# Performance work log

Hardware: AMD Instinct MI355X
Metric: run time of the kernel (lower is better)

Reference implementation:

```python
import jax, jax.numpy as jnp
import numpy as np

# Screen config (matches init_kwargs)
W, H, TL = 1920, 1080, 16
NBW = -(-W // TL)          # 120
NBH = -(-H // TL)          # 68
NB = NBW * NBH             # 8160 tiles
N = 500_000                # number of points
K = 5                      # max tiles per axis a point can overlap (radius < 24, TL=16)
RADIUS_MAX = 24.0


def setup_inputs() -> dict:
    key = jax.random.key(0)
    k1, k2, k3 = jax.random.split(key, 3)
    pos2d = jax.random.uniform(k1, (N, 2), dtype=jnp.float32) * jnp.array([W, H], dtype=jnp.float32)
    radius = jax.random.uniform(k2, (N,), dtype=jnp.float32) * (RADIUS_MAX - 1.0) + 1.0
    depth = jax.random.normal(k3, (N,), dtype=jnp.float32)
    return {"pos2d": pos2d, "radius": radius, "depth": depth}


def reference(pos2d, radius, depth):
    # Tile bounds per point (identical clamping semantics to the torch module).
    xmin = jnp.clip(jnp.floor_divide(pos2d[:, 0] - radius, TL), 0, NBW).astype(jnp.int32)
    ymin = jnp.clip(jnp.floor_divide(pos2d[:, 1] - radius, TL), 0, NBH).astype(jnp.int32)
    xmax = jnp.clip(jnp.floor_divide(pos2d[:, 0] + radius, TL) + 1, 0, NBW).astype(jnp.int32)
    ymax = jnp.clip(jnp.floor_divide(pos2d[:, 1] + radius, TL) + 1, 0, NBH).astype(jnp.int32)

    # Enumerate a fixed KxK candidate tile window per point, mask out-of-range tiles.
    dxy = jnp.arange(K, dtype=jnp.int32)
    xi = xmin[:, None] + dxy            # [N, K]
    yi = ymin[:, None] + dxy            # [N, K]
    vx = xi < xmax[:, None]
    vy = yi < ymax[:, None]
    valid = (vx[:, :, None] & vy[:, None, :]).reshape(-1)              # [E]
    tid = (xi[:, :, None] * NBH + yi[:, None, :]).reshape(-1)          # [E] flat tile id (x-major, as in module)
    tid = jnp.where(valid, tid, NB).astype(jnp.int32)                  # sentinel NB -> sorts to end
    pid = jnp.broadcast_to(jnp.arange(N, dtype=jnp.int32)[:, None, None], (N, K, K)).reshape(-1)
    d_entry = jnp.broadcast_to(depth[:, None, None], (N, K, K)).reshape(-1)

    # Counting-sort equivalent: per-tile histogram + exclusive cumsum offsets.
    counts = jax.ops.segment_sum(valid.astype(jnp.int32), tid, num_segments=NB + 1)[:NB]
    tile_count = jnp.concatenate([jnp.zeros((1,), jnp.int32), jnp.cumsum(counts)[:-1].astype(jnp.int32)])

    # Sort pairs by (tile id, depth descending) -> contiguous per-tile, depth-sorted index lists.
    order = jnp.lexsort((-d_entry, tid))
    tid_s = tid[order]
    pid_s = pid[order]
    live = tid_s < NB
    tile_indices = jnp.where(live, pid_s, -1)                          # padded with -1 at the tail
    sorted_depth = jnp.where(live, depth[pid_s], 0.0)                  # depths in per-tile sorted order
    return tile_count, tile_indices, sorted_depth
```

## Files before the change

### kernel.cpp

```cpp
#include <hip/hip_runtime.h>
#include <stdint.h>
#include <math.h>

typedef unsigned short u16;
typedef unsigned int u32;
typedef unsigned long long u64;

#define NBW 120
#define NBH 68
#define NTILES (NBW * NBH)
#define NPTS 500000
#define EE 12500000
#define SORT_CAP 768
#define NBKT 512
#define CAP 128
#define SLABF (NTILES * CAP * 2)
#define HB2 256
#define HT2 1024
#define RD_CH 8
#define RD_WB 17
#define DX 121
#define DY 69
#define DCELLS 8352
#define DCW (DCELLS / 2)

__device__ __forceinline__ int clampi(int v, int lo, int hi) {
    return v < lo ? lo : (v > hi ? hi : v);
}

__device__ __forceinline__ void tile_window(float x, float y, float r,
                                            int& x0, int& x1, int& y0, int& y1) {
    x0 = clampi((int)floorf((x - r) * 0.0625f), 0, NBW);
    x1 = clampi((int)floorf((x + r) * 0.0625f) + 1, 0, NBW);
    y0 = clampi((int)floorf((y - r) * 0.0625f), 0, NBH);
    y1 = clampi((int)floorf((y + r) * 0.0625f) + 1, 0, NBH);
}

__device__ __forceinline__ u32 depth_key(float d) {
    u32 fu = __float_as_uint(d);
    u32 asc = (fu & 0x80000000u) ? ~fu : (fu | 0x80000000u);
    return ~asc;
}
__device__ __forceinline__ float depth_unkey(u32 dk) {
    u32 asc = ~dk;
    u32 fu = (asc & 0x80000000u) ? (asc & 0x7FFFFFFFu) : ~asc;
    return __uint_as_float(fu);
}

__device__ __forceinline__ int tile_of_block(int b) {
    return (b & 7) * (NTILES / 8) + (b >> 3);
}

__device__ __forceinline__ u32 bucket_of(u32 dk, const u32* __restrict__ Ts) {
    u32 k = dk >> 24;
    u32 t0 = Ts[k], t1 = Ts[k + 1];
    u32 b = t0 + (((t1 - t0) * ((dk >> 8) & 0xFFFFu)) >> 16);
    return b >= NBKT ? (NBKT - 1) : b;
}

__device__ __forceinline__ void lds_inc16(u32* arr, int cell) {
    atomicAdd(&arr[cell >> 1], (cell & 1) ? 0x10000u : 1u);
}


__global__ void zero_kernel(u32* __restrict__ cnt, int* __restrict__ sdg) {
    int i = blockIdx.x * 1024 + threadIdx.x;
    if (i < NTILES) cnt[i] = 0;
    int j = i - NTILES;
    if (j >= 0 && j < DCELLS) sdg[j] = 0;
}

__global__ __launch_bounds__(HT2) void scatter_hist_kernel(const float2* __restrict__ pos,
                                                           const float* __restrict__ rad,
                                                           const float* __restrict__ depth,
                                                           u32* __restrict__ cnt,
                                                           u64* __restrict__ slab,
                                                           u32* __restrict__ diffslc) {
    __shared__ u32 s_dp[DCW];
    __shared__ u32 s_dm[DCW];
    int tid = threadIdx.x;
    for (int w = tid; w < DCW; w += HT2) { s_dp[w] = 0; s_dm[w] = 0; }
    __syncthreads();

    for (int i = blockIdx.x * HT2 + tid; i < NPTS; i += HB2 * HT2) {
        float2 p = pos[i];
        float r = rad[i];
        int x0, x1, y0, y1;
        tile_window(p.x, p.y, r, x0, x1, y0, y1);
        int cx = (int)(p.x * 0.0625f);
        int cy = (int)(p.y * 0.0625f);
        u32 dk = depth_key(depth[i]);
        u32 meta = ((u32)(cx - x0) << 11) | ((u32)(x1 - cx - 1) << 9)
                 | ((u32)y0 << 2) | (u32)(y1 - y0 - 1);
        int ct = cx * NBH + cy;
        u32 slot = atomicAdd(&cnt[ct], 1u);
        if (slot < CAP)
            slab[(size_t)ct * CAP + slot] = ((u64)dk << 32) | ((u64)(u32)i << 13) | (u64)meta;
        lds_inc16(s_dp, x0 * DY + y0);
        lds_inc16(s_dp, x1 * DY + y1);
        lds_inc16(s_dm, x0 * DY + y1);
        lds_inc16(s_dm, x1 * DY + y0);
    }
    __syncthreads();

    for (int wi = tid; wi < DCW; wi += HT2) {
        u32 pw = s_dp[wi], mw = s_dm[wi];
        int d0 = (int)(pw & 0xFFFFu) - (int)(mw & 0xFFFFu);
        int d1 = (int)(pw >> 16)     - (int)(mw >> 16);
        diffslc[blockIdx.x * DCW + wi] = ((u32)d0 & 0xFFFFu) | ((u32)d1 << 16);
    }
}

__global__ void reduce_diff_kernel(const u32* __restrict__ diffslc, int* __restrict__ sdg) {
    int chunk = blockIdx.x / RD_WB;
    int wb    = blockIdx.x % RD_WB;
    int wi = wb * 256 + threadIdx.x;
    if (wi >= DCW) return;
    int a0 = 0, a1 = 0;
    int b0 = chunk * (HB2 / RD_CH);
    for (int b = b0; b < b0 + HB2 / RD_CH; ++b) {
        u32 w = diffslc[b * DCW + wi];
        a0 += (int)(short)(w & 0xFFFFu);
        a1 += (int)(short)(w >> 16);
    }
    atomicAdd(&sdg[2 * wi],     a0);
    atomicAdd(&sdg[2 * wi + 1], a1);
}

__global__ __launch_bounds__(1024) void scan2_kernel(const int* __restrict__ sdg,
                                                     u32* __restrict__ eo,
                                                     float* __restrict__ out_count,
                                                     u32* __restrict__ Tg) {
    __shared__ int sd[DCELLS];
    __shared__ u32 wsum16[16];
    __shared__ u32 wpre[17];
    __shared__ u32 traw[257];
    int t = threadIdx.x;
    int lane = t & 63;
    int wvid = t >> 6;

    if (blockIdx.x == 0) {
        for (int c = t; c < DCELLS; c += 1024) sd[c] = sdg[c];
        __syncthreads();

        for (int x = wvid; x < DX; x += 16) {
            int idx = x * DY + lane;
            int v = sd[idx];
            for (int off = 1; off < 64; off <<= 1) {
                int n = __shfl_up(v, off, 64);
                if (lane >= off) v += n;
            }
            sd[idx] = v;
            int carry = __shfl(v, 63, 64);
            int y2 = 64 + lane;
            int v2 = (y2 < DY) ? sd[x * DY + y2] : 0;
            for (int off = 1; off < 64; off <<= 1) {
                int n = __shfl_up(v2, off, 64);
                if (lane >= off) v2 += n;
            }
            if (y2 < DY) sd[x * DY + y2] = v2 + carry;
        }
        __syncthreads();

        for (int y = wvid; y < DY; y += 16) {
            int idx = lane * DY + y;
            int v = sd[idx];
            for (int off = 1; off < 64; off <<= 1) {
                int n = __shfl_up(v, off, 64);
                if (lane >= off) v += n;
            }
            sd[idx] = v;
            int carry = __shfl(v, 63, 64);
            int x2 = 64 + lane;
            int v2 = (x2 < DX) ? sd[x2 * DY + y] : 0;
            for (int off = 1; off < 64; off <<= 1) {
                int n = __shfl_up(v2, off, 64);
                if (lane >= off) v2 += n;
            }
            if (x2 < DX) sd[x2 * DY + y] = v2 + carry;
        }
        __syncthreads();

        int base = t * 8;
        u32 local[8]; u32 sum = 0;
#pragma unroll
        for (int j = 0; j < 8; ++j) {
            int idx = base + j;
            u32 c = 0;
            if (idx < NTILES) {
                int x = idx / NBH, y = idx % NBH;
                c = (u32)sd[x * DY + y];
            }
            local[j] = c; sum += c;
        }
        u32 v = sum;
        for (int off = 1; off < 64; off <<= 1) {
            u32 n = __shfl_up(v, off, 64);
            if (lane >= off) v += n;
        }
        if (lane == 63) wsum16[wvid] = v;
        __syncthreads();
        if (t == 0) {
            u32 run = 0;
            wpre[0] = 0;
#pragma unroll
            for (int w = 0; w < 16; ++w) { run += wsum16[w]; wpre[w + 1] = run; }
        }
        __syncthreads();
        u32 run = wpre[wvid] + v - sum;
#pragma unroll
        for (int j = 0; j < 8; ++j) {
            int idx = base + j;
            if (idx < NTILES) {
                eo[idx] = run;
                out_count[idx] = (float)run;
                run += local[j];
            }
        }
        if (t == 1023) eo[NTILES] = wpre[16];
    } else {
        if (t < 257) {
            u32 dkb = (u32)t << 24;
            float d = depth_unkey(dkb);
            float u;
            if (d != d) u = (t < 128) ? 0.f : 1.f;
            else {
                float dc = fminf(fmaxf(d, -12.f), 12.f);
                u = 0.5f * erfcf(dc * 0.70710678f);
            }
            traw[t] = (u32)(u * (float)NBKT + 0.5f);
        }
        __syncthreads();
        if (t == 0) {
            u32 run = 0;
            for (int k = 0; k < 257; ++k) {
                u32 v = traw[k];
                if (v > NBKT) v = NBKT;
                if (v > run) run = v;
                Tg[k] = run;
            }
        }
    }
}

__global__ __launch_bounds__(256) void tile_build_kernel(const u32* __restrict__ cnt,
                                                         const u64* __restrict__ slab,
                                                         const u32* __restrict__ eo,
                                                         const u32* __restrict__ Tg,
                                                         float* __restrict__ out_idx,
                                                         float* __restrict__ out_depth) {
    __shared__ u64 keys[SORT_CAP];
    __shared__ u64 keys2[SORT_CAP];
    __shared__ u32 boff[NBKT + 1];
    __shared__ u32 bcur[NBKT];
    __shared__ u32 Ts[257];
    __shared__ u32 wsum[4];
    __shared__ u32 lcnt;
    __shared__ u32 nb_n[25];
    __shared__ u32 nb_base[25];
    __shared__ int nb_dcx[25];

    int tid = threadIdx.x;
    int lane = tid & 63;
    int wv = tid >> 6;

    {
        u32 total = eo[NTILES];
        u32 tailn = EE - total;
        u32 per = (tailn + NTILES - 1) / NTILES;
        u64 s = (u64)total + (u64)blockIdx.x * per;
        u64 e = s + per; if (e > (u64)EE) e = EE;
        for (u64 i = s + tid; i < e; i += 256) out_idx[i] = -1.f;

        u32 limit = EE - SLABF;
        u32 tn2 = limit > total ? limit - total : 0;
        u32 per2 = (tn2 + NTILES - 1) / NTILES;
        u64 s2 = (u64)total + (u64)blockIdx.x * per2;
        u64 e2 = s2 + per2; if (e2 > (u64)limit) e2 = limit;
        for (u64 i = s2 + tid; i < e2; i += 256) out_depth[i] = 0.f;
    }

    int t = tile_of_block(blockIdx.x);
    u32 base = eo[t];
    int cnt_e = (int)(eo[t + 1] - base);
    if (cnt_e <= 0) return;

    int tx = t / NBH;
    int ty = t % NBH;
    bool big = cnt_e > SORT_CAP;

    for (int b = tid; b < NBKT; b += 256) boff[b] = 0;
    for (int k = tid; k < 257; k += 256) Ts[k] = Tg[k];
    if (tid == 0) lcnt = 0;
    if (tid < 25) {
        int dx = tid / 5 - 2, dy = tid % 5 - 2;
        int ncx = tx + dx, ncy = ty + dy;
        u32 n = 0, b = 0;
        if (ncx >= 0 && ncx < NBW && ncy >= 0 && ncy < NBH) {
            int nt = ncx * NBH + ncy;
            n = cnt[nt]; if (n > CAP) n = CAP;
            b = (u32)nt * CAP;
        }
        nb_base[tid] = b;
        nb_dcx[tid] = dx;
        nb_n[tid] = n;
    }
    __syncthreads();

    if (!big) {
        for (int k = wv; k < 25; k += 4) {
            u32 n = nb_n[k];
            if (!n) continue;
            const u64* sp = slab + nb_base[k];
            int dcx = nb_dcx[k];
            for (u32 j0 = 0; j0 < n; j0 += 64) {
                u32 j = j0 + lane;
                bool acc = false;
                u64 v = 0;
                if (j < n) {
                    v = sp[j];
                    u32 meta = (u32)v & 0x1FFFu;
                    int h = (int)(meta & 3u);
                    int y0 = (int)((meta >> 2) & 127u);
                    int dx1m1 = (int)((meta >> 9) & 3u);
                    int dx0 = (int)((meta >> 11) & 3u);
                    acc = (dx0 >= dcx && dx1m1 >= -dcx && ty >= y0 && ty <= y0 + h);
                }
                u64 mask = __ballot(acc);
                if (!mask) continue;
                int leader = __ffsll((unsigned long long)mask) - 1;
                u32 nacc = (u32)__popcll(mask);
                u32 wbase = 0;
                if (lane == leader) wbase = atomicAdd(&lcnt, nacc);
                wbase = __shfl(wbase, leader, 64);
                if (acc) {
                    u32 rank = (u32)__popcll(mask & ((1ull << lane) - 1ull));
                    keys[wbase + rank] = v;
                    atomicAdd(&boff[bucket_of((u32)(v >> 32), Ts)], 1u);
                }
            }
        }
        __syncthreads();

        {
            int b0 = tid * 2;
            u32 h0 = boff[b0], h1 = boff[b0 + 1];
            u32 tsum = h0 + h1;
            u32 v = tsum;
            for (int off = 1; off < 64; off <<= 1) {
                u32 n = __shfl_up(v, off, 64);
                if (lane >= off) v += n;
            }
            if (lane == 63) wsum[wv] = v;
            __syncthreads();
            u32 wpre = 0;
            for (int w = 0; w < wv; ++w) wpre += wsum[w];
            u32 run = wpre + v - tsum;
            boff[b0] = run;     bcur[b0] = run;     run += h0;
            boff[b0 + 1] = run; bcur[b0 + 1] = run; run += h1;
            if (tid == 255) boff[NBKT] = run;
        }
        __syncthreads();

        for (int i = tid; i < cnt_e; i += 256) {
            u64 v = keys[i];
            u32 slot = atomicAdd(&bcur[bucket_of((u32)(v >> 32), Ts)], 1u);
            keys2[slot] = v;
        }
        __syncthreads();

        for (int b = tid; b < NBKT; b += 256) {
            int s = (int)boff[b], e = (int)boff[b + 1];
            for (int i = s + 1; i < e; ++i) {
                u64 k = keys2[i];
                int j = i - 1;
                while (j >= s && keys2[j] > k) { keys2[j + 1] = keys2[j]; --j; }
                keys2[j + 1] = k;
            }
        }
        __syncthreads();

        for (int i = tid; i < cnt_e; i += 256) {
            u64 k = keys2[i];
            u32 pid = (u32)(k >> 13) & 0x7FFFFu;
            u32 dk  = (u32)(k >> 32);
            out_idx[base + i]   = (float)pid;
            out_depth[base + i] = depth_unkey(dk);
        }
    } else {
        for (int k = wv; k < 25; k += 4) {
            u32 n = nb_n[k];
            if (!n) continue;
            const u64* sp = slab + nb_base[k];
            int dcx = nb_dcx[k];
            for (u32 j = lane; j < n; j += 64) {
                u64 v = sp[j];
                u32 meta = (u32)v & 0x1FFFu;
                int h = (int)(meta & 3u);
                int y0 = (int)((meta >> 2) & 127u);
                int dx1m1 = (int)((meta >> 9) & 3u);
                int dx0 = (int)((meta >> 11) & 3u);
                if (dx0 >= dcx && dx1m1 >= -dcx && ty >= y0 && ty <= y0 + h) {
                    u32 pid = (u32)(v >> 13) & 0x7FFFFu;
                    u32 dk  = (u32)(v >> 32);
                    u32 slot = atomicAdd(&lcnt, 1u);
                    out_idx[base + slot] = (float)pid;
                    out_depth[base + slot] = depth_unkey(dk);
                }
            }
        }
        __syncthreads();
        for (int round = 0; round < cnt_e; ++round) {
            for (int i = (round & 1) + 2 * tid; i + 1 < cnt_e; i += 512) {
                float fi0 = out_idx[base + i], fi1 = out_idx[base + i + 1];
                float fd0 = out_depth[base + i], fd1 = out_depth[base + i + 1];
                u64 k0 = ((u64)depth_key(fd0) << 19) | (u64)(u32)fi0;
                u64 k1 = ((u64)depth_key(fd1) << 19) | (u64)(u32)fi1;
                if (k0 > k1) {
                    out_idx[base + i] = fi1; out_idx[base + i + 1] = fi0;
                    out_depth[base + i] = fd1; out_depth[base + i + 1] = fd0;
                }
            }
            __syncthreads();
        }
    }
}

__global__ void zero_slab_kernel(float4* __restrict__ dst) {
    int n = SLABF / 4;
    for (int i = blockIdx.x * 256 + threadIdx.x; i < n; i += 512 * 256)
        dst[i] = make_float4(0.f, 0.f, 0.f, 0.f);
}

extern "C" void kernel_launch(void* const* d_in, const int* in_sizes, int n_in,
                              void* d_out, int out_size, void* d_ws, size_t ws_size,
                              hipStream_t stream) {
    (void)in_sizes; (void)n_in; (void)out_size; (void)ws_size;

    const float2* pos  = (const float2*)d_in[0];
    const float* rad   = (const float*)d_in[1];
    const float* depth = (const float*)d_in[2];

    float* out        = (float*)d_out;
    float* out_count  = out;
    float* out_idx    = out + NTILES;
    float* out_depth  = out + NTILES + EE;

    u32* cnt     = (u32*)d_ws;
    u32* eo      = cnt + NTILES;
    int* sdg     = (int*)(eo + NTILES + 1);
    u32* Tg      = (u32*)(sdg + DCELLS);

    u64* slab    = (u64*)(out_depth + EE) - (size_t)NTILES * CAP;
    u32* diffslc = (u32*)(out_idx + EE) - (size_t)HB2 * DCW;

    zero_kernel<<<(NTILES + DCELLS + 1023) / 1024, 1024, 0, stream>>>(cnt, sdg);
    scatter_hist_kernel<<<HB2, HT2, 0, stream>>>(pos, rad, depth, cnt, slab, diffslc);
    reduce_diff_kernel<<<RD_CH * RD_WB, 256, 0, stream>>>(diffslc, sdg);
    scan2_kernel<<<2, 1024, 0, stream>>>(sdg, eo, out_count, Tg);
    tile_build_kernel<<<NTILES, 256, 0, stream>>>(cnt, slab, eo, Tg, out_idx, out_depth);
    zero_slab_kernel<<<512, 256, 0, stream>>>((float4*)(out_depth + EE - SLABF));
}
```

Baseline: 207.2 us.

## Replace center-tile slab gather with atomic per-tile scatter into output

Removes the per-point center-tile slab and the 25-neighbour gather in tile_build. A new expand kernel scatters each point's (pid, depth) straight into its tiles' output ranges using global atomic cursors seeded from the prefix scan. tile_build then reads those unsorted entries back and sorts them in place. It also drops the zero and zero_slab kernels and reworks the histogram grid to one point per thread. The cost is about 4.5M global atomics and scattered writes, plus an extra read-back pass.

After: 321.0 us. +54.9%, slower.

```diff
diff --git a/kernel.cpp b/kernel.cpp
--- a/kernel.cpp
+++ b/kernel.cpp
@@ -13,12 +13,12 @@
 #define EE 12500000
 #define SORT_CAP 768
 #define NBKT 512
-#define CAP 128
-#define SLABF (NTILES * CAP * 2)
-#define HB2 256
-#define HT2 1024
-#define RD_CH 8
+#define HB 512
+#define HT 1024
+#define PB 1024
+#define PT 512
 #define RD_WB 17
+#define RD_CH 16
 #define DX 121
 #define DY 69
 #define DCELLS 8352
@@ -47,10 +47,6 @@
     return __uint_as_float(fu);
 }
 
-__device__ __forceinline__ int tile_of_block(int b) {
-    return (b & 7) * (NTILES / 8) + (b >> 3);
-}
-
 __device__ __forceinline__ u32 bucket_of(u32 dk, const u32* __restrict__ Ts) {
     u32 k = dk >> 24;
     u32 t0 = Ts[k], t1 = Ts[k + 1];
@@ -62,40 +58,26 @@
     atomicAdd(&arr[cell >> 1], (cell & 1) ? 0x10000u : 1u);
 }
 
-
-__global__ void zero_kernel(u32* __restrict__ cnt, int* __restrict__ sdg) {
-    int i = blockIdx.x * 1024 + threadIdx.x;
-    if (i < NTILES) cnt[i] = 0;
-    int j = i - NTILES;
-    if (j >= 0 && j < DCELLS) sdg[j] = 0;
-}
-
-__global__ __launch_bounds__(HT2) void scatter_hist_kernel(const float2* __restrict__ pos,
-                                                           const float* __restrict__ rad,
-                                                           const float* __restrict__ depth,
-                                                           u32* __restrict__ cnt,
-                                                           u64* __restrict__ slab,
-                                                           u32* __restrict__ diffslc) {
+__global__ __launch_bounds__(HT) void hist_kernel(const float2* __restrict__ pos,
+                                                  const float* __restrict__ rad,
+                                                  u32* __restrict__ diffslc,
+                                                  int* __restrict__ sdg) {
     __shared__ u32 s_dp[DCW];
     __shared__ u32 s_dm[DCW];
     int tid = threadIdx.x;
-    for (int w = tid; w < DCW; w += HT2) { s_dp[w] = 0; s_dm[w] = 0; }
+    for (int w = tid; w < DCW; w += HT) { s_dp[w] = 0; s_dm[w] = 0; }
+    if (blockIdx.x < 9) {
+        int j = blockIdx.x * HT + tid;
+        if (j < DCELLS) sdg[j] = 0;
+    }
     __syncthreads();
 
-    for (int i = blockIdx.x * HT2 + tid; i < NPTS; i += HB2 * HT2) {
+    int i = blockIdx.x * HT + tid;
+    if (i < NPTS) {
         float2 p = pos[i];
         float r = rad[i];
         int x0, x1, y0, y1;
         tile_window(p.x, p.y, r, x0, x1, y0, y1);
-        int cx = (int)(p.x * 0.0625f);
-        int cy = (int)(p.y * 0.0625f);
-        u32 dk = depth_key(depth[i]);
-        u32 meta = ((u32)(cx - x0) << 11) | ((u32)(x1 - cx - 1) << 9)
-                 | ((u32)y0 << 2) | (u32)(y1 - y0 - 1);
-        int ct = cx * NBH + cy;
-        u32 slot = atomicAdd(&cnt[ct], 1u);
-        if (slot < CAP)
-            slab[(size_t)ct * CAP + slot] = ((u64)dk << 32) | ((u64)(u32)i << 13) | (u64)meta;
         lds_inc16(s_dp, x0 * DY + y0);
         lds_inc16(s_dp, x1 * DY + y1);
         lds_inc16(s_dm, x0 * DY + y1);
@@ -103,7 +85,7 @@
     }
     __syncthreads();
 
-    for (int wi = tid; wi < DCW; wi += HT2) {
+    for (int wi = tid; wi < DCW; wi += HT) {
         u32 pw = s_dp[wi], mw = s_dm[wi];
         int d0 = (int)(pw & 0xFFFFu) - (int)(mw & 0xFFFFu);
         int d1 = (int)(pw >> 16)     - (int)(mw >> 16);
@@ -117,8 +99,8 @@
     int wi = wb * 256 + threadIdx.x;
     if (wi >= DCW) return;
     int a0 = 0, a1 = 0;
-    int b0 = chunk * (HB2 / RD_CH);
-    for (int b = b0; b < b0 + HB2 / RD_CH; ++b) {
+    int b0 = chunk * (HB / RD_CH);
+    for (int b = b0; b < b0 + HB / RD_CH; ++b) {
         u32 w = diffslc[b * DCW + wi];
         a0 += (int)(short)(w & 0xFFFFu);
         a1 += (int)(short)(w >> 16);
@@ -129,6 +111,7 @@
 
 __global__ __launch_bounds__(1024) void scan2_kernel(const int* __restrict__ sdg,
                                                      u32* __restrict__ eo,
+                                                     u32* __restrict__ ecur,
                                                      float* __restrict__ out_count,
                                                      u32* __restrict__ Tg) {
     __shared__ int sd[DCELLS];
@@ -213,6 +196,7 @@
             int idx = base + j;
             if (idx < NTILES) {
                 eo[idx] = run;
+                ecur[idx] = run;
                 out_count[idx] = (float)run;
                 run += local[j];
             }
@@ -243,9 +227,31 @@
     }
 }
 
-__global__ __launch_bounds__(256) void tile_build_kernel(const u32* __restrict__ cnt,
-                                                         const u64* __restrict__ slab,
-                                                         const u32* __restrict__ eo,
+__global__ __launch_bounds__(PT) void expand_kernel(const float2* __restrict__ pos,
+                                                    const float* __restrict__ rad,
+                                                    const float* __restrict__ depth,
+                                                    u32* __restrict__ ecur,
+                                                    float* __restrict__ out_idx,
+                                                    float* __restrict__ out_depth) {
+    int i = blockIdx.x * PT + threadIdx.x;
+    if (i >= NPTS) return;
+    float2 p = pos[i];
+    float r = rad[i];
+    float d = depth[i];
+    int x0, x1, y0, y1;
+    tile_window(p.x, p.y, r, x0, x1, y0, y1);
+    float fpid = (float)i;
+    for (int ix = x0; ix < x1; ++ix) {
+        int rowb = ix * NBH;
+        for (int iy = y0; iy < y1; ++iy) {
+            u32 slot = atomicAdd(&ecur[rowb + iy], 1u);
+            out_idx[slot]   = fpid;
+            out_depth[slot] = d;
+        }
+    }
+}
+
+__global__ __launch_bounds__(256) void tile_build_kernel(const u32* __restrict__ eo,
                                                          const u32* __restrict__ Tg,
                                                          float* __restrict__ out_idx,
                                                          float* __restrict__ out_depth) {
@@ -255,10 +261,6 @@
     __shared__ u32 bcur[NBKT];
     __shared__ u32 Ts[257];
     __shared__ u32 wsum[4];
-    __shared__ u32 lcnt;
-    __shared__ u32 nb_n[25];
-    __shared__ u32 nb_base[25];
-    __shared__ int nb_dcx[25];
 
     int tid = threadIdx.x;
     int lane = tid & 63;
@@ -270,75 +272,28 @@
         u32 per = (tailn + NTILES - 1) / NTILES;
         u64 s = (u64)total + (u64)blockIdx.x * per;
         u64 e = s + per; if (e > (u64)EE) e = EE;
-        for (u64 i = s + tid; i < e; i += 256) out_idx[i] = -1.f;
-
-        u32 limit = EE - SLABF;
-        u32 tn2 = limit > total ? limit - total : 0;
-        u32 per2 = (tn2 + NTILES - 1) / NTILES;
-        u64 s2 = (u64)total + (u64)blockIdx.x * per2;
-        u64 e2 = s2 + per2; if (e2 > (u64)limit) e2 = limit;
-        for (u64 i = s2 + tid; i < e2; i += 256) out_depth[i] = 0.f;
-    }
-
-    int t = tile_of_block(blockIdx.x);
+        for (u64 i = s + tid; i < e; i += 256) {
+            out_idx[i] = -1.f;
+            out_depth[i] = 0.f;
+        }
+    }
+
+    int t = blockIdx.x;
     u32 base = eo[t];
     int cnt_e = (int)(eo[t + 1] - base);
     if (cnt_e <= 0) return;
 
-    int tx = t / NBH;
-    int ty = t % NBH;
-    bool big = cnt_e > SORT_CAP;
-
     for (int b = tid; b < NBKT; b += 256) boff[b] = 0;
     for (int k = tid; k < 257; k += 256) Ts[k] = Tg[k];
-    if (tid == 0) lcnt = 0;
-    if (tid < 25) {
-        int dx = tid / 5 - 2, dy = tid % 5 - 2;
-        int ncx = tx + dx, ncy = ty + dy;
-        u32 n = 0, b = 0;
-        if (ncx >= 0 && ncx < NBW && ncy >= 0 && ncy < NBH) {
-            int nt = ncx * NBH + ncy;
-            n = cnt[nt]; if (n > CAP) n = CAP;
-            b = (u32)nt * CAP;
-        }
-        nb_base[tid] = b;
-        nb_dcx[tid] = dx;
-        nb_n[tid] = n;
-    }
     __syncthreads();
 
-    if (!big) {
-        for (int k = wv; k < 25; k += 4) {
-            u32 n = nb_n[k];
-            if (!n) continue;
-            const u64* sp = slab + nb_base[k];
-            int dcx = nb_dcx[k];
-            for (u32 j0 = 0; j0 < n; j0 += 64) {
-                u32 j = j0 + lane;
-                bool acc = false;
-                u64 v = 0;
-                if (j < n) {
-                    v = sp[j];
-                    u32 meta = (u32)v & 0x1FFFu;
-                    int h = (int)(meta & 3u);
-                    int y0 = (int)((meta >> 2) & 127u);
-                    int dx1m1 = (int)((meta >> 9) & 3u);
-                    int dx0 = (int)((meta >> 11) & 3u);
-                    acc = (dx0 >= dcx && dx1m1 >= -dcx && ty >= y0 && ty <= y0 + h);
-                }
-                u64 mask = __ballot(acc);
-                if (!mask) continue;
-                int leader = __ffsll((unsigned long long)mask) - 1;
-                u32 nacc = (u32)__popcll(mask);
-                u32 wbase = 0;
-                if (lane == leader) wbase = atomicAdd(&lcnt, nacc);
-                wbase = __shfl(wbase, leader, 64);
-                if (acc) {
-                    u32 rank = (u32)__popcll(mask & ((1ull << lane) - 1ull));
-                    keys[wbase + rank] = v;
-                    atomicAdd(&boff[bucket_of((u32)(v >> 32), Ts)], 1u);
-                }
-            }
+    if (cnt_e <= SORT_CAP) {
+        for (int i = tid; i < cnt_e; i += 256) {
+            float fi = out_idx[base + i];
+            float fd = out_depth[base + i];
+            u32 dk = depth_key(fd);
+            keys[i] = ((u64)dk << 19) | (u64)(u32)fi;
+            atomicAdd(&boff[bucket_of(dk, Ts)], 1u);
         }
         __syncthreads();
 
@@ -364,7 +319,7 @@
 
         for (int i = tid; i < cnt_e; i += 256) {
             u64 v = keys[i];
-            u32 slot = atomicAdd(&bcur[bucket_of((u32)(v >> 32), Ts)], 1u);
+            u32 slot = atomicAdd(&bcur[bucket_of((u32)(v >> 19), Ts)], 1u);
             keys2[slot] = v;
         }
         __syncthreads();
@@ -382,34 +337,10 @@
 
         for (int i = tid; i < cnt_e; i += 256) {
             u64 k = keys2[i];
-            u32 pid = (u32)(k >> 13) & 0x7FFFFu;
-            u32 dk  = (u32)(k >> 32);
-            out_idx[base + i]   = (float)pid;
-            out_depth[base + i] = depth_unkey(dk);
+            out_idx[base + i]   = (float)(u32)(k & 0x7FFFFu);
+            out_depth[base + i] = depth_unkey((u32)(k >> 19));
         }
     } else {
-        for (int k = wv; k < 25; k += 4) {
-            u32 n = nb_n[k];
-            if (!n) continue;
-            const u64* sp = slab + nb_base[k];
-            int dcx = nb_dcx[k];
-            for (u32 j = lane; j < n; j += 64) {
-                u64 v = sp[j];
-                u32 meta = (u32)v & 0x1FFFu;
-                int h = (int)(meta & 3u);
-                int y0 = (int)((meta >> 2) & 127u);
-                int dx1m1 = (int)((meta >> 9) & 3u);
-                int dx0 = (int)((meta >> 11) & 3u);
-                if (dx0 >= dcx && dx1m1 >= -dcx && ty >= y0 && ty <= y0 + h) {
-                    u32 pid = (u32)(v >> 13) & 0x7FFFFu;
-                    u32 dk  = (u32)(v >> 32);
-                    u32 slot = atomicAdd(&lcnt, 1u);
-                    out_idx[base + slot] = (float)pid;
-                    out_depth[base + slot] = depth_unkey(dk);
-                }
-            }
-        }
-        __syncthreads();
         for (int round = 0; round < cnt_e; ++round) {
             for (int i = (round & 1) + 2 * tid; i + 1 < cnt_e; i += 512) {
                 float fi0 = out_idx[base + i], fi1 = out_idx[base + i + 1];
@@ -426,12 +357,6 @@
     }
 }
 
-__global__ void zero_slab_kernel(float4* __restrict__ dst) {
-    int n = SLABF / 4;
-    for (int i = blockIdx.x * 256 + threadIdx.x; i < n; i += 512 * 256)
-        dst[i] = make_float4(0.f, 0.f, 0.f, 0.f);
-}
-
 extern "C" void kernel_launch(void* const* d_in, const int* in_sizes, int n_in,
                               void* d_out, int out_size, void* d_ws, size_t ws_size,
                               hipStream_t stream) {
@@ -446,18 +371,16 @@
     float* out_idx    = out + NTILES;
     float* out_depth  = out + NTILES + EE;
 
-    u32* cnt     = (u32*)d_ws;
-    u32* eo      = cnt + NTILES;
-    int* sdg     = (int*)(eo + NTILES + 1);
-    u32* Tg      = (u32*)(sdg + DCELLS);
-
-    u64* slab    = (u64*)(out_depth + EE) - (size_t)NTILES * CAP;
-    u32* diffslc = (u32*)(out_idx + EE) - (size_t)HB2 * DCW;
-
-    zero_kernel<<<(NTILES + DCELLS + 1023) / 1024, 1024, 0, stream>>>(cnt, sdg);
-    scatter_hist_kernel<<<HB2, HT2, 0, stream>>>(pos, rad, depth, cnt, slab, diffslc);
+    u32* eo   = (u32*)d_ws;
+    u32* ecur = eo + NTILES + 1;
+    int* sdg  = (int*)(ecur + NTILES);
+    u32* Tg   = (u32*)(sdg + DCELLS);
+
+    u32* diffslc = (u32*)(out_idx + EE) - (size_t)HB * DCW;
+
+    hist_kernel<<<HB, HT, 0, stream>>>(pos, rad, diffslc, sdg);
     reduce_diff_kernel<<<RD_CH * RD_WB, 256, 0, stream>>>(diffslc, sdg);
-    scan2_kernel<<<2, 1024, 0, stream>>>(sdg, eo, out_count, Tg);
-    tile_build_kernel<<<NTILES, 256, 0, stream>>>(cnt, slab, eo, Tg, out_idx, out_depth);
-    zero_slab_kernel<<<512, 256, 0, stream>>>((float4*)(out_depth + EE - SLABF));
-}
+    scan2_kernel<<<2, 1024, 0, stream>>>(sdg, eo, ecur, out_count, Tg);
+    expand_kernel<<<PB, PT, 0, stream>>>(pos, rad, depth, ecur, out_idx, out_depth);
+    tile_build_kernel<<<NTILES, 256, 0, stream>>>(eo, Tg, out_idx, out_depth);
+}
```

## Move tail padding fill into a dedicated vectorized kernel and rebalance histogram grid

Applied to the files above, without the earlier changes.

Removes the per-block scalar tail fill of out_idx (-1) and out_depth (0) from tile_build_kernel and the separate slab-zeroing kernel, replacing both with one float4-vectorized pad_fill kernel that runs after tile building. The zeroing of the diff grid sdg moves into the scatter kernel, and the scatter grid changes from 256x1024 to 512x512 threads with more reduce chunks. This is meant to cut scalar strided stores and a launch, at the cost of an extra full pass over the padded tail of both output arrays. Because the slab scratch lives in the out_depth tail, the fill has to run last so the scratch gets overwritten.

After: 211.2 us. No clear change (+1.9%).

```diff
diff --git a/kernel.cpp b/kernel.cpp
--- a/kernel.cpp
+++ b/kernel.cpp
@@ -14,10 +14,9 @@
 #define SORT_CAP 768
 #define NBKT 512
 #define CAP 128
-#define SLABF (NTILES * CAP * 2)
-#define HB2 256
-#define HT2 1024
-#define RD_CH 8
+#define HB2 512
+#define HT2 512
+#define RD_CH 16
 #define RD_WB 17
 #define DX 121
 #define DY 69
@@ -63,11 +62,9 @@
 }
 
 
-__global__ void zero_kernel(u32* __restrict__ cnt, int* __restrict__ sdg) {
+__global__ void zero_kernel(u32* __restrict__ cnt) {
     int i = blockIdx.x * 1024 + threadIdx.x;
     if (i < NTILES) cnt[i] = 0;
-    int j = i - NTILES;
-    if (j >= 0 && j < DCELLS) sdg[j] = 0;
 }
 
 __global__ __launch_bounds__(HT2) void scatter_hist_kernel(const float2* __restrict__ pos,
@@ -75,11 +72,16 @@
                                                            const float* __restrict__ depth,
                                                            u32* __restrict__ cnt,
                                                            u64* __restrict__ slab,
-                                                           u32* __restrict__ diffslc) {
+                                                           u32* __restrict__ diffslc,
+                                                           int* __restrict__ sdg) {
     __shared__ u32 s_dp[DCW];
     __shared__ u32 s_dm[DCW];
     int tid = threadIdx.x;
     for (int w = tid; w < DCW; w += HT2) { s_dp[w] = 0; s_dm[w] = 0; }
+    if (blockIdx.x < 17) {
+        int j = blockIdx.x * HT2 + tid;
+        if (j < DCELLS) sdg[j] = 0;
+    }
     __syncthreads();
 
     for (int i = blockIdx.x * HT2 + tid; i < NPTS; i += HB2 * HT2) {
@@ -263,22 +265,6 @@
     int tid = threadIdx.x;
     int lane = tid & 63;
     int wv = tid >> 6;
-
-    {
-        u32 total = eo[NTILES];
-        u32 tailn = EE - total;
-        u32 per = (tailn + NTILES - 1) / NTILES;
-        u64 s = (u64)total + (u64)blockIdx.x * per;
-        u64 e = s + per; if (e > (u64)EE) e = EE;
-        for (u64 i = s + tid; i < e; i += 256) out_idx[i] = -1.f;
-
-        u32 limit = EE - SLABF;
-        u32 tn2 = limit > total ? limit - total : 0;
-        u32 per2 = (tn2 + NTILES - 1) / NTILES;
-        u64 s2 = (u64)total + (u64)blockIdx.x * per2;
-        u64 e2 = s2 + per2; if (e2 > (u64)limit) e2 = limit;
-        for (u64 i = s2 + tid; i < e2; i += 256) out_depth[i] = 0.f;
-    }
 
     int t = tile_of_block(blockIdx.x);
     u32 base = eo[t];
@@ -426,10 +412,27 @@
     }
 }
 
-__global__ void zero_slab_kernel(float4* __restrict__ dst) {
-    int n = SLABF / 4;
-    for (int i = blockIdx.x * 256 + threadIdx.x; i < n; i += 512 * 256)
-        dst[i] = make_float4(0.f, 0.f, 0.f, 0.f);
+__global__ __launch_bounds__(256) void pad_fill_kernel(const u32* __restrict__ eo,
+                                                       float* __restrict__ out_idx,
+                                                       float* __restrict__ out_depth) {
+    u32 total = eo[NTILES];
+    u64 gtid = (u64)blockIdx.x * 256 + threadIdx.x;
+    u64 nthr = (u64)gridDim.x * 256;
+
+    u64 a4 = ((u64)total + 3) & ~3ull;
+    if (gtid < a4 - total) {
+        out_idx[total + gtid] = -1.f;
+        out_depth[total + gtid] = 0.f;
+    }
+    u64 n4 = ((u64)EE - a4) >> 2;
+    float4* p_i = (float4*)(out_idx + a4);
+    float4* p_d = (float4*)(out_depth + a4);
+    float4 vi = make_float4(-1.f, -1.f, -1.f, -1.f);
+    float4 vd = make_float4(0.f, 0.f, 0.f, 0.f);
+    for (u64 i = gtid; i < n4; i += nthr) {
+        p_i[i] = vi;
+        p_d[i] = vd;
+    }
 }
 
 extern "C" void kernel_launch(void* const* d_in, const int* in_sizes, int n_in,
@@ -446,18 +449,18 @@
     float* out_idx    = out + NTILES;
     float* out_depth  = out + NTILES + EE;
 
-    u32* cnt     = (u32*)d_ws;
-    u32* eo      = cnt + NTILES;
-    int* sdg     = (int*)(eo + NTILES + 1);
-    u32* Tg      = (u32*)(sdg + DCELLS);
+    u32* cnt = (u32*)d_ws;
+    u32* eo  = cnt + NTILES;
+    int* sdg = (int*)(eo + NTILES + 1);
+    u32* Tg  = (u32*)(sdg + DCELLS);
 
     u64* slab    = (u64*)(out_depth + EE) - (size_t)NTILES * CAP;
     u32* diffslc = (u32*)(out_idx + EE) - (size_t)HB2 * DCW;
 
-    zero_kernel<<<(NTILES + DCELLS + 1023) / 1024, 1024, 0, stream>>>(cnt, sdg);
-    scatter_hist_kernel<<<HB2, HT2, 0, stream>>>(pos, rad, depth, cnt, slab, diffslc);
+    zero_kernel<<<8, 1024, 0, stream>>>(cnt);
+    scatter_hist_kernel<<<HB2, HT2, 0, stream>>>(pos, rad, depth, cnt, slab, diffslc, sdg);
     reduce_diff_kernel<<<RD_CH * RD_WB, 256, 0, stream>>>(diffslc, sdg);
     scan2_kernel<<<2, 1024, 0, stream>>>(sdg, eo, out_count, Tg);
     tile_build_kernel<<<NTILES, 256, 0, stream>>>(cnt, slab, eo, Tg, out_idx, out_depth);
-    zero_slab_kernel<<<512, 256, 0, stream>>>((float4*)(out_depth + EE - SLABF));
-}
+    pad_fill_kernel<<<2048, 256, 0, stream>>>(eo, out_idx, out_depth);
+}
```

## Fuse reduce and scan via last-block ticket, move slab to workspace

Applied to the files above, without the earlier changes.

The Tg table build moves into the init kernel, and the diff-reduction and 2D prefix-scan kernels merge into one launch where the last block to finish, found by an atomic ticket, performs the scan with 256 threads. When the workspace is large enough, the per-tile slab lives there instead of in the output tail, so the trailing zero_slab kernel is skipped and tile_build zero-fills the whole depth tail itself. This cuts launches and serial dependencies. The price is a scan run by a single 256-thread block, and a reduction split into twice as many chunks with more atomics.

Measured after the change: 242.8 us. 1.17x slower.

```diff
diff --git a/kernel.cpp b/kernel.cpp
--- a/kernel.cpp
+++ b/kernel.cpp
@@ -14,11 +14,13 @@
 #define SORT_CAP 768
 #define NBKT 512
 #define CAP 128
+#define SLABN ((size_t)NTILES * CAP)
 #define SLABF (NTILES * CAP * 2)
 #define HB2 256
 #define HT2 1024
-#define RD_CH 8
+#define RD_CH 16
 #define RD_WB 17
+#define RD_BLOCKS (RD_CH * RD_WB)
 #define DX 121
 #define DY 69
 #define DCELLS 8352
@@ -63,11 +65,40 @@
 }
 
 
-__global__ void zero_kernel(u32* __restrict__ cnt, int* __restrict__ sdg) {
-    int i = blockIdx.x * 1024 + threadIdx.x;
-    if (i < NTILES) cnt[i] = 0;
-    int j = i - NTILES;
-    if (j >= 0 && j < DCELLS) sdg[j] = 0;
+__global__ __launch_bounds__(1024) void init_kernel(u32* __restrict__ cnt,
+                                                    int* __restrict__ sdg,
+                                                    u32* __restrict__ done,
+                                                    u32* __restrict__ Tg) {
+    __shared__ u32 traw[257];
+    int t = threadIdx.x;
+    int gid = blockIdx.x * 1024 + t;
+    if (gid < NTILES) cnt[gid] = 0;
+    else if (gid - NTILES < DCELLS) sdg[gid - NTILES] = 0;
+    if (gid == NTILES + DCELLS) *done = 0;
+
+    if (blockIdx.x == 16) {
+        if (t < 257) {
+            u32 dkb = (u32)t << 24;
+            float d = depth_unkey(dkb);
+            float u;
+            if (d != d) u = (t < 128) ? 0.f : 1.f;
+            else {
+                float dc = fminf(fmaxf(d, -12.f), 12.f);
+                u = 0.5f * erfcf(dc * 0.70710678f);
+            }
+            traw[t] = (u32)(u * (float)NBKT + 0.5f);
+        }
+        __syncthreads();
+        if (t == 0) {
+            u32 run = 0;
+            for (int k = 0; k < 257; ++k) {
+                u32 v = traw[k];
+                if (v > NBKT) v = NBKT;
+                if (v > run) run = v;
+                Tg[k] = run;
+            }
+        }
+    }
 }
 
 __global__ __launch_bounds__(HT2) void scatter_hist_kernel(const float2* __restrict__ pos,
@@ -111,136 +142,108 @@
     }
 }
 
-__global__ void reduce_diff_kernel(const u32* __restrict__ diffslc, int* __restrict__ sdg) {
-    int chunk = blockIdx.x / RD_WB;
-    int wb    = blockIdx.x % RD_WB;
-    int wi = wb * 256 + threadIdx.x;
-    if (wi >= DCW) return;
-    int a0 = 0, a1 = 0;
-    int b0 = chunk * (HB2 / RD_CH);
-    for (int b = b0; b < b0 + HB2 / RD_CH; ++b) {
-        u32 w = diffslc[b * DCW + wi];
-        a0 += (int)(short)(w & 0xFFFFu);
-        a1 += (int)(short)(w >> 16);
-    }
-    atomicAdd(&sdg[2 * wi],     a0);
-    atomicAdd(&sdg[2 * wi + 1], a1);
-}
-
-__global__ __launch_bounds__(1024) void scan2_kernel(const int* __restrict__ sdg,
-                                                     u32* __restrict__ eo,
-                                                     float* __restrict__ out_count,
-                                                     u32* __restrict__ Tg) {
+__global__ __launch_bounds__(256) void reduce_scan_kernel(const u32* __restrict__ diffslc,
+                                                          int* __restrict__ sdg,
+                                                          u32* __restrict__ done,
+                                                          u32* __restrict__ eo,
+                                                          float* __restrict__ out_count) {
     __shared__ int sd[DCELLS];
-    __shared__ u32 wsum16[16];
-    __shared__ u32 wpre[17];
-    __shared__ u32 traw[257];
+    __shared__ u32 wsum[4];
+    __shared__ u32 tick_s;
     int t = threadIdx.x;
     int lane = t & 63;
-    int wvid = t >> 6;
-
-    if (blockIdx.x == 0) {
-        for (int c = t; c < DCELLS; c += 1024) sd[c] = sdg[c];
-        __syncthreads();
-
-        for (int x = wvid; x < DX; x += 16) {
-            int idx = x * DY + lane;
-            int v = sd[idx];
-            for (int off = 1; off < 64; off <<= 1) {
-                int n = __shfl_up(v, off, 64);
-                if (lane >= off) v += n;
-            }
-            sd[idx] = v;
-            int carry = __shfl(v, 63, 64);
-            int y2 = 64 + lane;
-            int v2 = (y2 < DY) ? sd[x * DY + y2] : 0;
-            for (int off = 1; off < 64; off <<= 1) {
-                int n = __shfl_up(v2, off, 64);
-                if (lane >= off) v2 += n;
-            }
-            if (y2 < DY) sd[x * DY + y2] = v2 + carry;
-        }
-        __syncthreads();
-
-        for (int y = wvid; y < DY; y += 16) {
-            int idx = lane * DY + y;
-            int v = sd[idx];
-            for (int off = 1; off < 64; off <<= 1) {
-                int n = __shfl_up(v, off, 64);
-                if (lane >= off) v += n;
-            }
-            sd[idx] = v;
-            int carry = __shfl(v, 63, 64);
-            int x2 = 64 + lane;
-            int v2 = (x2 < DX) ? sd[x2 * DY + y] : 0;
-            for (int off = 1; off < 64; off <<= 1) {
-                int n = __shfl_up(v2, off, 64);
-                if (lane >= off) v2 += n;
-            }
-            if (x2 < DX) sd[x2 * DY + y] = v2 + carry;
-        }
-        __syncthreads();
-
-        int base = t * 8;
-        u32 local[8]; u32 sum = 0;
-#pragma unroll
-        for (int j = 0; j < 8; ++j) {
-            int idx = base + j;
-            u32 c = 0;
-            if (idx < NTILES) {
-                int x = idx / NBH, y = idx % NBH;
-                c = (u32)sd[x * DY + y];
-            }
-            local[j] = c; sum += c;
-        }
-        u32 v = sum;
+    int wv = t >> 6;
+
+    {
+        int chunk = blockIdx.x / RD_WB;
+        int wb    = blockIdx.x % RD_WB;
+        int wi = wb * 256 + t;
+        if (wi < DCW) {
+            int a0 = 0, a1 = 0;
+            int b0 = chunk * (HB2 / RD_CH);
+            for (int b = b0; b < b0 + HB2 / RD_CH; ++b) {
+                u32 w = diffslc[b * DCW + wi];
+                a0 += (int)(short)(w & 0xFFFFu);
+                a1 += (int)(short)(w >> 16);
+            }
+            atomicAdd(&sdg[2 * wi],     a0);
+            atomicAdd(&sdg[2 * wi + 1], a1);
+        }
+    }
+    __threadfence();
+    __syncthreads();
+    if (t == 0) tick_s = atomicAdd(done, 1u);
+    __syncthreads();
+    if (tick_s != RD_BLOCKS - 1) return;
+
+    for (int c = t; c < DCELLS; c += 256) sd[c] = atomicAdd(&sdg[c], 0);
+    __syncthreads();
+
+    for (int x = wv; x < DX; x += 4) {
+        int v = sd[x * DY + lane];
         for (int off = 1; off < 64; off <<= 1) {
-            u32 n = __shfl_up(v, off, 64);
+            int n = __shfl_up(v, off, 64);
             if (lane >= off) v += n;
         }
-        if (lane == 63) wsum16[wvid] = v;
-        __syncthreads();
-        if (t == 0) {
-            u32 run = 0;
-            wpre[0] = 0;
-#pragma unroll
-            for (int w = 0; w < 16; ++w) { run += wsum16[w]; wpre[w + 1] = run; }
-        }
-        __syncthreads();
-        u32 run = wpre[wvid] + v - sum;
-#pragma unroll
-        for (int j = 0; j < 8; ++j) {
-            int idx = base + j;
-            if (idx < NTILES) {
-                eo[idx] = run;
-                out_count[idx] = (float)run;
-                run += local[j];
-            }
-        }
-        if (t == 1023) eo[NTILES] = wpre[16];
-    } else {
-        if (t < 257) {
-            u32 dkb = (u32)t << 24;
-            float d = depth_unkey(dkb);
-            float u;
-            if (d != d) u = (t < 128) ? 0.f : 1.f;
-            else {
-                float dc = fminf(fmaxf(d, -12.f), 12.f);
-                u = 0.5f * erfcf(dc * 0.70710678f);
-            }
-            traw[t] = (u32)(u * (float)NBKT + 0.5f);
-        }
-        __syncthreads();
-        if (t == 0) {
-            u32 run = 0;
-            for (int k = 0; k < 257; ++k) {
-                u32 v = traw[k];
-                if (v > NBKT) v = NBKT;
-                if (v > run) run = v;
-                Tg[k] = run;
-            }
-        }
-    }
+        sd[x * DY + lane] = v;
+        int carry = __shfl(v, 63, 64);
+        int y2 = 64 + lane;
+        int v2 = (y2 < DY) ? sd[x * DY + y2] : 0;
+        for (int off = 1; off < 64; off <<= 1) {
+            int n = __shfl_up(v2, off, 64);
+            if (lane >= off) v2 += n;
+        }
+        if (y2 < DY) sd[x * DY + y2] = v2 + carry;
+    }
+    __syncthreads();
+
+    for (int y = wv; y < DY; y += 4) {
+        int v = sd[lane * DY + y];
+        for (int off = 1; off < 64; off <<= 1) {
+            int n = __shfl_up(v, off, 64);
+            if (lane >= off) v += n;
+        }
+        sd[lane * DY + y] = v;
+        int carry = __shfl(v, 63, 64);
+        int x2 = 64 + lane;
+        int v2 = (x2 < DX) ? sd[x2 * DY + y] : 0;
+        for (int off = 1; off < 64; off <<= 1) {
+            int n = __shfl_up(v2, off, 64);
+            if (lane >= off) v2 += n;
+        }
+        if (x2 < DX) sd[x2 * DY + y] = v2 + carry;
+    }
+    __syncthreads();
+
+    int base = t * 32;
+    u32 sum = 0;
+    for (int j = 0; j < 32; ++j) {
+        int idx = base + j;
+        if (idx < NTILES) {
+            int x = idx / NBH, y = idx - x * NBH;
+            sum += (u32)sd[x * DY + y];
+        }
+    }
+    u32 v = sum;
+    for (int off = 1; off < 64; off <<= 1) {
+        u32 n = __shfl_up(v, off, 64);
+        if (lane >= off) v += n;
+    }
+    if (lane == 63) wsum[wv] = v;
+    __syncthreads();
+    u32 wpre = 0;
+    for (int w = 0; w < wv; ++w) wpre += wsum[w];
+    u32 run = wpre + v - sum;
+    for (int j = 0; j < 32; ++j) {
+        int idx = base + j;
+        if (idx < NTILES) {
+            int x = idx / NBH, y = idx - x * NBH;
+            eo[idx] = run;
+            out_count[idx] = (float)run;
+            run += (u32)sd[x * DY + y];
+        }
+    }
+    if (t == 255) eo[NTILES] = run;
 }
 
 __global__ __launch_bounds__(256) void tile_build_kernel(const u32* __restrict__ cnt,
@@ -248,7 +251,8 @@
                                                          const u32* __restrict__ eo,
                                                          const u32* __restrict__ Tg,
                                                          float* __restrict__ out_idx,
-                                                         float* __restrict__ out_depth) {
+                                                         float* __restrict__ out_depth,
+                                                         u32 depth_fill_end) {
     __shared__ u64 keys[SORT_CAP];
     __shared__ u64 keys2[SORT_CAP];
     __shared__ u32 boff[NBKT + 1];
@@ -272,7 +276,7 @@
         u64 e = s + per; if (e > (u64)EE) e = EE;
         for (u64 i = s + tid; i < e; i += 256) out_idx[i] = -1.f;
 
-        u32 limit = EE - SLABF;
+        u32 limit = depth_fill_end;
         u32 tn2 = limit > total ? limit - total : 0;
         u32 per2 = (tn2 + NTILES - 1) / NTILES;
         u64 s2 = (u64)total + (u64)blockIdx.x * per2;
@@ -435,7 +439,7 @@
 extern "C" void kernel_launch(void* const* d_in, const int* in_sizes, int n_in,
                               void* d_out, int out_size, void* d_ws, size_t ws_size,
                               hipStream_t stream) {
-    (void)in_sizes; (void)n_in; (void)out_size; (void)ws_size;
+    (void)in_sizes; (void)n_in; (void)out_size;
 
     const float2* pos  = (const float2*)d_in[0];
     const float* rad   = (const float*)d_in[1];
@@ -446,18 +450,35 @@
     float* out_idx    = out + NTILES;
     float* out_depth  = out + NTILES + EE;
 
-    u32* cnt     = (u32*)d_ws;
-    u32* eo      = cnt + NTILES;
-    int* sdg     = (int*)(eo + NTILES + 1);
-    u32* Tg      = (u32*)(sdg + DCELLS);
-
-    u64* slab    = (u64*)(out_depth + EE) - (size_t)NTILES * CAP;
+    const size_t small_bytes = (size_t)NTILES * 4
+                             + (size_t)(NTILES + 1) * 4
+                             + (size_t)DCELLS * 4
+                             + 257 * 4 + 4;
+    const size_t slab_bytes = SLABN * 8;
+    bool slab_in_ws = ws_size >= slab_bytes + small_bytes;
+
+    u64* slab;
+    u32* cnt;
+    if (slab_in_ws) {
+        slab = (u64*)d_ws;
+        cnt  = (u32*)(slab + SLABN);
+    } else {
+        slab = (u64*)(out_depth + EE) - SLABN;
+        cnt  = (u32*)d_ws;
+    }
+    u32* eo   = cnt + NTILES;
+    int* sdg  = (int*)(eo + NTILES + 1);
+    u32* Tg   = (u32*)(sdg + DCELLS);
+    u32* done = Tg + 257;
+
     u32* diffslc = (u32*)(out_idx + EE) - (size_t)HB2 * DCW;
 
-    zero_kernel<<<(NTILES + DCELLS + 1023) / 1024, 1024, 0, stream>>>(cnt, sdg);
+    u32 dfe = slab_in_ws ? (u32)EE : (u32)(EE - SLABF);
+
+    init_kernel<<<17, 1024, 0, stream>>>(cnt, sdg, done, Tg);
     scatter_hist_kernel<<<HB2, HT2, 0, stream>>>(pos, rad, depth, cnt, slab, diffslc);
-    reduce_diff_kernel<<<RD_CH * RD_WB, 256, 0, stream>>>(diffslc, sdg);
-    scan2_kernel<<<2, 1024, 0, stream>>>(sdg, eo, out_count, Tg);
-    tile_build_kernel<<<NTILES, 256, 0, stream>>>(cnt, slab, eo, Tg, out_idx, out_depth);
-    zero_slab_kernel<<<512, 256, 0, stream>>>((float4*)(out_depth + EE - SLABF));
-}
+    reduce_scan_kernel<<<RD_BLOCKS, 256, 0, stream>>>(diffslc, sdg, done, eo, out_count);
+    tile_build_kernel<<<NTILES, 256, 0, stream>>>(cnt, slab, eo, Tg, out_idx, out_depth, dfe);
+    if (!slab_in_ws)
+        zero_slab_kernel<<<512, 256, 0, stream>>>((float4*)(out_depth + EE - SLABF));
+}
```
